# Optimization experiments

Measured on AMD Instinct MI355X. Metric: run time of the kernel, lower is better.

Reference implementation:

```python
import jax, jax.numpy as jnp
import numpy as np

N, E, D_IN, D_HID, D_OUT = 50000, 600000, 128, 128, 64


def setup_inputs() -> dict:
    key = jax.random.key(0)
    ks = jax.random.split(key, 8)
    x = jax.random.normal(ks[0], (N, D_IN), dtype=jnp.float32)
    edge_index = jax.random.randint(ks[1], (2, E), 0, N, dtype=jnp.int64)
    def glorot(k, fan_in, fan_out):
        s = (6.0 / (fan_in + fan_out)) ** 0.5
        return jax.random.uniform(k, (fan_in, fan_out), jnp.float32, -s, s)
    return {
        "x": x,
        "W1": glorot(ks[2], D_IN, D_HID), "b1": jnp.zeros((D_HID,), jnp.float32),
        "W2": glorot(ks[3], D_HID, D_HID), "b2": jnp.zeros((D_HID,), jnp.float32),
        "W3": glorot(ks[4], D_HID, D_OUT), "b3": jnp.zeros((D_OUT,), jnp.float32),
        "edge_index": edge_index,
    }


def reference(x, W1, b1, W2, b2, W3, b3, edge_index):
    n = x.shape[0]
    # GCN with self-loops: A_hat = A + I, norm = D^-1/2 A_hat D^-1/2
    loops = jnp.arange(n, dtype=edge_index.dtype)
    row = jnp.concatenate([edge_index[0], loops])  # source nodes
    col = jnp.concatenate([edge_index[1], loops])  # target nodes
    deg = jax.ops.segment_sum(jnp.ones_like(col, dtype=x.dtype), col, num_segments=n)
    dinv = jnp.where(deg > 0, jax.lax.rsqrt(deg), 0.0)
    norm = dinv[row] * dinv[col]  # [E+N]

    def gcn_conv(h, W, b):
        hw = h @ W                                   # [N, out]
        msg = hw[row] * norm[:, None]                # [E+N, out] gather + scale
        return jax.ops.segment_sum(msg, col, num_segments=n) + b

    h = jax.nn.relu(gcn_conv(x, W1, b1))
    h = jax.nn.relu(gcn_conv(h, W2, b2))
    return gcn_conv(h, W3, b3)
```

## Files before the change

kernel.cpp:

```cpp
#include <hip/hip_runtime.h>
#include <hip/hip_bf16.h>
#include <hip/hip_fp16.h>


typedef _Float16 h2 __attribute__((ext_vector_type(2)));
typedef _Float16 h8 __attribute__((ext_vector_type(8)));

__device__ inline float4 h4_to_f4(float2 raw) {
    __half2 lo = *reinterpret_cast<__half2*>(&raw.x);
    __half2 hi = *reinterpret_cast<__half2*>(&raw.y);
    float2 a = __half22float2(lo);
    float2 b = __half22float2(hi);
    return make_float4(a.x, a.y, b.x, b.y);
}

__device__ inline uint pack_h2(float a, float b) {
    __half2 h = __floats2half2_rn(a, b);
    return *reinterpret_cast<uint*>(&h);
}

__global__ __launch_bounds__(256) void zero_counts_kernel(int4* __restrict__ p, int n4) {
    int i = blockIdx.x * 256 + threadIdx.x;
    if (i < n4) p[i] = make_int4(0, 0, 0, 0);
}

__global__ __launch_bounds__(256) void f32_to_f16_kernel(const float4* __restrict__ in,
                                                         uint2* __restrict__ out, int n4) {
    int i = blockIdx.x * 256 + threadIdx.x;
    if (i < n4) {
        float4 v = in[i];
        out[i] = make_uint2(pack_h2(v.x, v.y), pack_h2(v.z, v.w));
    }
}

__global__ void count_edges_kernel(const int* __restrict__ col, int* __restrict__ counts, int E) {
    int e = blockIdx.x * blockDim.x + threadIdx.x;
    if (e < E) atomicAdd(&counts[col[e]], 1);
}

__global__ __launch_bounds__(256) void block_sum_kernel(const int* __restrict__ counts,
                                                        int* __restrict__ blocksum, int n) {
    int i = blockIdx.x * 256 + threadIdx.x;
    int v = (i < n) ? counts[i] : 0;
    #pragma unroll
    for (int d = 1; d < 64; d <<= 1) v += __shfl_xor(v, d);
    __shared__ int ws[4];
    if ((threadIdx.x & 63) == 0) ws[threadIdx.x >> 6] = v;
    __syncthreads();
    if (threadIdx.x == 0) blocksum[blockIdx.x] = ws[0] + ws[1] + ws[2] + ws[3];
}

__global__ __launch_bounds__(256) void scan_sums_kernel(const int* __restrict__ blocksum,
                                                        int* __restrict__ blockoff,
                                                        int* __restrict__ offsets, int nb, int n) {
    int tid = threadIdx.x;
    int lane = tid & 63, wid = tid >> 6;
    int orig = (tid < nb) ? blocksum[tid] : 0;
    int v = orig;
    #pragma unroll
    for (int d = 1; d < 64; d <<= 1) {
        int u = __shfl_up(v, d);
        if (lane >= d) v += u;
    }
    __shared__ int ws[4];
    if (lane == 63) ws[wid] = v;
    __syncthreads();
    int add = 0;
    for (int w = 0; w < wid; ++w) add += ws[w];
    v += add;
    if (tid < nb) blockoff[tid] = v - orig;
    if (tid == 255) offsets[n] = v;
}

__global__ __launch_bounds__(256) void write_offsets_kernel(const int* __restrict__ counts,
                                                            const int* __restrict__ blockoff,
                                                            int* __restrict__ offsets,
                                                            int* __restrict__ cursor,
                                                            float* __restrict__ dinv, int n) {
    int tid = threadIdx.x;
    int i = blockIdx.x * 256 + tid;
    int lane = tid & 63, wid = tid >> 6;
    int c = (i < n) ? counts[i] : 0;
    int v = c;
    #pragma unroll
    for (int d = 1; d < 64; d <<= 1) {
        int u = __shfl_up(v, d);
        if (lane >= d) v += u;
    }
    __shared__ int ws[4];
    if (lane == 63) ws[wid] = v;
    __syncthreads();
    int add = 0;
    for (int w = 0; w < wid; ++w) add += ws[w];
    int incl = v + add;
    if (i < n) {
        offsets[i] = blockoff[blockIdx.x] + incl - c;
        cursor[i] = 0;
        dinv[i] = rsqrtf((float)(c + 1));
    }
}

__global__ void fill_csr_kernel(const int* __restrict__ row, const int* __restrict__ col,
                                const int* __restrict__ offsets, int* __restrict__ cursor,
                                int* __restrict__ srcs, int E) {
    int e = blockIdx.x * blockDim.x + threadIdx.x;
    if (e < E) {
        int c = col[e];
        int pos = offsets[c] + atomicAdd(&cursor[c], 1);
        srcs[pos] = row[e];
    }
}

template <int DO>
__global__ __launch_bounds__(256) void gemm16_kernel(const __half* __restrict__ A,
                                                     const float* __restrict__ W,
                                                     const float* __restrict__ dinv,
                                                     __half* __restrict__ out, int n) {
    constexpr int K = 128;
    constexpr int COLTH = DO / 8;
    constexpr int ROWTH = 256 / COLTH;
    constexpr int R = 64 / ROWTH;
    constexpr int BR = ROWTH * R;
    constexpr int HALF = DO / 2;

    __shared__ alignas(16) h2 Wl[(K / 2) * DO];

    int tid = threadIdx.x;
    for (int idx = tid; idx < (K / 2) * (DO / 4); idx += 256) {
        int k2 = idx / (DO / 4);
        int c4 = idx % (DO / 4);
        float4 w0 = ((const float4*)(W + (size_t)(2 * k2) * DO))[c4];
        float4 w1 = ((const float4*)(W + (size_t)(2 * k2 + 1) * DO))[c4];
        h2* dst = &Wl[k2 * DO + c4 * 4];
        h2 d0; d0.x = (_Float16)w0.x; d0.y = (_Float16)w1.x; dst[0] = d0;
        h2 d1; d1.x = (_Float16)w0.y; d1.y = (_Float16)w1.y; dst[1] = d1;
        h2 d2; d2.x = (_Float16)w0.z; d2.y = (_Float16)w1.z; dst[2] = d2;
        h2 d3; d3.x = (_Float16)w0.w; d3.y = (_Float16)w1.w; dst[3] = d3;
    }
    __syncthreads();

    int ct = tid % COLTH;
    int rt = tid / COLTH;
    int rb = blockIdx.x * BR + rt * R;

    int rowc[R];
    #pragma unroll
    for (int i = 0; i < R; ++i) {
        int row = rb + i;
        rowc[i] = (row < n) ? row : (n - 1);
    }

    float acc[R][8];
    #pragma unroll
    for (int i = 0; i < R; ++i)
        #pragma unroll
        for (int c = 0; c < 8; ++c) acc[i][c] = 0.f;

    #pragma unroll 2
    for (int k8 = 0; k8 < K / 8; ++k8) {
        h8 av[R];
        #pragma unroll
        for (int i = 0; i < R; ++i) {
            av[i] = ((const h8*)(A + (size_t)rowc[i] * K))[k8];
        }
        #pragma unroll
        for (int kk = 0; kk < 4; ++kk) {
            int k2 = k8 * 4 + kk;
            h2 w0[4], w1[4];
            *(uint4*)w0 = *(const uint4*)(&Wl[k2 * DO + ct * 4]);
            *(uint4*)w1 = *(const uint4*)(&Wl[k2 * DO + HALF + ct * 4]);
            #pragma unroll
            for (int i = 0; i < R; ++i) {
                h2 a; a.x = av[i][2 * kk]; a.y = av[i][2 * kk + 1];
                #pragma unroll
                for (int c = 0; c < 4; ++c) {
                    acc[i][c]     = __builtin_amdgcn_fdot2(a, w0[c], acc[i][c], false);
                    acc[i][4 + c] = __builtin_amdgcn_fdot2(a, w1[c], acc[i][4 + c], false);
                }
            }
        }
    }

    #pragma unroll
    for (int i = 0; i < R; ++i) {
        int row = rb + i;
        if (row < n) {
            float dv = dinv[row];
            uint2 q0 = make_uint2(pack_h2(acc[i][0] * dv, acc[i][1] * dv),
                                  pack_h2(acc[i][2] * dv, acc[i][3] * dv));
            uint2 q1 = make_uint2(pack_h2(acc[i][4] * dv, acc[i][5] * dv),
                                  pack_h2(acc[i][6] * dv, acc[i][7] * dv));
            *(uint2*)(out + (size_t)row * DO + ct * 4) = q0;
            *(uint2*)(out + (size_t)row * DO + HALF + ct * 4) = q1;
        }
    }
}

template <int DO, bool RELU, bool F16OUT>
__global__ __launch_bounds__(256) void agg_kernel(const __half* __restrict__ hw,
                                                  const int* __restrict__ offsets,
                                                  const int* __restrict__ srcs,
                                                  const float* __restrict__ dinv,
                                                  const float* __restrict__ bias,
                                                  void* __restrict__ outp, int n) {
    constexpr int TPD = DO / 4;
    constexpr int DPB = 256 / TPD;
    int d = blockIdx.x * DPB + threadIdx.x / TPD;
    int j = threadIdx.x % TPD;
    if (d >= n) return;

    const float2* hw2 = (const float2*)hw;
    int beg = offsets[d];
    int end = offsets[d + 1];

    float4 acc = h4_to_f4(hw2[(size_t)d * TPD + j]);

    int e = beg;
    for (; e + 8 <= end; e += 8) {
        int s0 = srcs[e + 0], s1 = srcs[e + 1], s2 = srcs[e + 2], s3 = srcs[e + 3];
        int s4 = srcs[e + 4], s5 = srcs[e + 5], s6 = srcs[e + 6], s7 = srcs[e + 7];
        float4 v0 = h4_to_f4(hw2[(size_t)s0 * TPD + j]);
        float4 v1 = h4_to_f4(hw2[(size_t)s1 * TPD + j]);
        float4 v2 = h4_to_f4(hw2[(size_t)s2 * TPD + j]);
        float4 v3 = h4_to_f4(hw2[(size_t)s3 * TPD + j]);
        float4 v4 = h4_to_f4(hw2[(size_t)s4 * TPD + j]);
        float4 v5 = h4_to_f4(hw2[(size_t)s5 * TPD + j]);
        float4 v6 = h4_to_f4(hw2[(size_t)s6 * TPD + j]);
        float4 v7 = h4_to_f4(hw2[(size_t)s7 * TPD + j]);
        acc.x += v0.x; acc.y += v0.y; acc.z += v0.z; acc.w += v0.w;
        acc.x += v1.x; acc.y += v1.y; acc.z += v1.z; acc.w += v1.w;
        acc.x += v2.x; acc.y += v2.y; acc.z += v2.z; acc.w += v2.w;
        acc.x += v3.x; acc.y += v3.y; acc.z += v3.z; acc.w += v3.w;
        acc.x += v4.x; acc.y += v4.y; acc.z += v4.z; acc.w += v4.w;
        acc.x += v5.x; acc.y += v5.y; acc.z += v5.z; acc.w += v5.w;
        acc.x += v6.x; acc.y += v6.y; acc.z += v6.z; acc.w += v6.w;
        acc.x += v7.x; acc.y += v7.y; acc.z += v7.z; acc.w += v7.w;
    }
    for (; e + 4 <= end; e += 4) {
        int s0 = srcs[e + 0], s1 = srcs[e + 1], s2 = srcs[e + 2], s3 = srcs[e + 3];
        float4 v0 = h4_to_f4(hw2[(size_t)s0 * TPD + j]);
        float4 v1 = h4_to_f4(hw2[(size_t)s1 * TPD + j]);
        float4 v2 = h4_to_f4(hw2[(size_t)s2 * TPD + j]);
        float4 v3 = h4_to_f4(hw2[(size_t)s3 * TPD + j]);
        acc.x += v0.x; acc.y += v0.y; acc.z += v0.z; acc.w += v0.w;
        acc.x += v1.x; acc.y += v1.y; acc.z += v1.z; acc.w += v1.w;
        acc.x += v2.x; acc.y += v2.y; acc.z += v2.z; acc.w += v2.w;
        acc.x += v3.x; acc.y += v3.y; acc.z += v3.z; acc.w += v3.w;
    }
    for (; e < end; ++e) {
        float4 v = h4_to_f4(hw2[(size_t)srcs[e] * TPD + j]);
        acc.x += v.x; acc.y += v.y; acc.z += v.z; acc.w += v.w;
    }

    float di = dinv[d];
    float4 b4 = ((const float4*)bias)[j];
    acc.x = b4.x + di * acc.x;
    acc.y = b4.y + di * acc.y;
    acc.z = b4.z + di * acc.z;
    acc.w = b4.w + di * acc.w;

    if (RELU) {
        acc.x = fmaxf(acc.x, 0.f); acc.y = fmaxf(acc.y, 0.f);
        acc.z = fmaxf(acc.z, 0.f); acc.w = fmaxf(acc.w, 0.f);
    }
    if (F16OUT) {
        uint2 q = make_uint2(pack_h2(acc.x, acc.y), pack_h2(acc.z, acc.w));
        ((uint2*)outp)[(size_t)d * TPD + j] = q;
    } else {
        ((float4*)outp)[(size_t)d * TPD + j] = acc;
    }
}

extern "C" void kernel_launch(void* const* d_in, const int* in_sizes, int n_in,
                              void* d_out, int out_size, void* d_ws, size_t ws_size,
                              hipStream_t stream) {
    const float* x  = (const float*)d_in[0];
    const float* W1 = (const float*)d_in[1];
    const float* b1 = (const float*)d_in[2];
    const float* W2 = (const float*)d_in[3];
    const float* b2 = (const float*)d_in[4];
    const float* W3 = (const float*)d_in[5];
    const float* b3 = (const float*)d_in[6];
    const int*   ei = (const int*)d_in[7];

    const int N = in_sizes[0] / 128;
    const int E = in_sizes[7] / 2;
    const int* rowi = ei;
    const int* coli = ei + E;

    float* out = (float*)d_out;

    char* ws = (char*)d_ws;
    size_t off = 0;
    auto alloc = [&](size_t bytes) -> void* {
        void* p = ws + off;
        off = (off + bytes + 255) & ~(size_t)255;
        return p;
    };
    const int NB = (N + 255) / 256;
    float* dinv     = (float*)alloc((size_t)N * 4);
    int*   counts   = (int*)  alloc(((size_t)N + 4) * 4);
    int*   offsets  = (int*)  alloc((size_t)(N + 1) * 4);
    int*   cursor   = (int*)  alloc((size_t)N * 4);
    int*   blocksum = (int*)  alloc((size_t)NB * 4);
    int*   blockoff = (int*)  alloc((size_t)NB * 4);
    int*   srcs     = (int*)  alloc((size_t)E * 4);
    __half* x16     = (__half*)alloc((size_t)N * 128 * 2);
    __half* hw16    = (__half*)alloc((size_t)N * 128 * 2);
    __half* h16     = (__half*)alloc((size_t)N * 128 * 2);

    const int n4 = (N + 3) / 4;
    zero_counts_kernel<<<(n4 + 255) / 256, 256, 0, stream>>>((int4*)counts, n4);
    count_edges_kernel<<<(E + 255) / 256, 256, 0, stream>>>(coli, counts, E);
    block_sum_kernel<<<NB, 256, 0, stream>>>(counts, blocksum, N);
    scan_sums_kernel<<<1, 256, 0, stream>>>(blocksum, blockoff, offsets, NB, N);
    write_offsets_kernel<<<NB, 256, 0, stream>>>(counts, blockoff, offsets, cursor, dinv, N);
    fill_csr_kernel<<<(E + 255) / 256, 256, 0, stream>>>(rowi, coli, offsets, cursor, srcs, E);
    const int xc4 = N * 128 / 4;
    f32_to_f16_kernel<<<(xc4 + 255) / 256, 256, 0, stream>>>((const float4*)x, (uint2*)x16, xc4);

    gemm16_kernel<128><<<(N + 63) / 64, 256, 0, stream>>>(x16, W1, dinv, hw16, N);
    agg_kernel<128, true, true><<<(N + 7) / 8, 256, 0, stream>>>(hw16, offsets, srcs, dinv, b1, h16, N);

    gemm16_kernel<128><<<(N + 63) / 64, 256, 0, stream>>>(h16, W2, dinv, hw16, N);
    agg_kernel<128, true, true><<<(N + 7) / 8, 256, 0, stream>>>(hw16, offsets, srcs, dinv, b2, h16, N);

    gemm16_kernel<64><<<(N + 63) / 64, 256, 0, stream>>>(h16, W3, dinv, hw16, N);
    agg_kernel<64, false, false><<<(N + 15) / 16, 256, 0, stream>>>(hw16, offsets, srcs, dinv, b3, out, N);
}
```

Baseline: 215.7 us.

## Fuse prelude kernels, single-pass decoupled scan, and prefetch source indices in aggregation

Merges zeroing of the edge counts and the fp32-to-fp16 conversion of x into one kernel. Replaces the three-kernel offsets scan with a single-pass scan in which each block publishes its total to a flag slot and spins on all earlier slots. The aggregation loop now loads the next eight source indices while the current gathers are in flight. Together these cut the number of kernel launches and hide index-load latency, at the cost of relying on forward progress of earlier blocks for the spin-wait.

```diff
diff --git a/kernel.cpp b/kernel.cpp
--- a/kernel.cpp
+++ b/kernel.cpp
@@ -19,17 +19,17 @@
     return *reinterpret_cast<uint*>(&h);
 }
 
-__global__ __launch_bounds__(256) void zero_counts_kernel(int4* __restrict__ p, int n4) {
+__global__ __launch_bounds__(256) void prelude_init_kernel(const float4* __restrict__ x,
+                                                           uint2* __restrict__ x16,
+                                                           int4* __restrict__ counts4, int n4,
+                                                           int* __restrict__ aggslot, int nb,
+                                                           int xc4) {
     int i = blockIdx.x * 256 + threadIdx.x;
-    if (i < n4) p[i] = make_int4(0, 0, 0, 0);
-}
-
-__global__ __launch_bounds__(256) void f32_to_f16_kernel(const float4* __restrict__ in,
-                                                         uint2* __restrict__ out, int n4) {
-    int i = blockIdx.x * 256 + threadIdx.x;
-    if (i < n4) {
-        float4 v = in[i];
-        out[i] = make_uint2(pack_h2(v.x, v.y), pack_h2(v.z, v.w));
+    if (i < n4) counts4[i] = make_int4(0, 0, 0, 0);
+    if (i < nb) aggslot[i] = -1;
+    if (i < xc4) {
+        float4 v = x[i];
+        x16[i] = make_uint2(pack_h2(v.x, v.y), pack_h2(v.z, v.w));
     }
 }
 
@@ -38,66 +38,52 @@
     if (e < E) atomicAdd(&counts[col[e]], 1);
 }
 
-__global__ __launch_bounds__(256) void block_sum_kernel(const int* __restrict__ counts,
-                                                        int* __restrict__ blocksum, int n) {
-    int i = blockIdx.x * 256 + threadIdx.x;
-    int v = (i < n) ? counts[i] : 0;
-    #pragma unroll
-    for (int d = 1; d < 64; d <<= 1) v += __shfl_xor(v, d);
-    __shared__ int ws[4];
-    if ((threadIdx.x & 63) == 0) ws[threadIdx.x >> 6] = v;
-    __syncthreads();
-    if (threadIdx.x == 0) blocksum[blockIdx.x] = ws[0] + ws[1] + ws[2] + ws[3];
-}
-
-__global__ __launch_bounds__(256) void scan_sums_kernel(const int* __restrict__ blocksum,
-                                                        int* __restrict__ blockoff,
-                                                        int* __restrict__ offsets, int nb, int n) {
+__global__ __launch_bounds__(256) void scan_fused_kernel(const int* __restrict__ counts,
+                                                         int* __restrict__ aggslot,
+                                                         int* __restrict__ offsets,
+                                                         int* __restrict__ cursor,
+                                                         float* __restrict__ dinv, int n) {
+    int b = blockIdx.x;
     int tid = threadIdx.x;
     int lane = tid & 63, wid = tid >> 6;
-    int orig = (tid < nb) ? blocksum[tid] : 0;
-    int v = orig;
+    int i = b * 256 + tid;
+    int c = (i < n) ? counts[i] : 0;
+
+    int s = c;
     #pragma unroll
     for (int d = 1; d < 64; d <<= 1) {
-        int u = __shfl_up(v, d);
-        if (lane >= d) v += u;
+        int u = __shfl_up(s, d);
+        if (lane >= d) s += u;
     }
     __shared__ int ws[4];
-    if (lane == 63) ws[wid] = v;
+    if (lane == 63) ws[wid] = s;
     __syncthreads();
     int add = 0;
     for (int w = 0; w < wid; ++w) add += ws[w];
-    v += add;
-    if (tid < nb) blockoff[tid] = v - orig;
-    if (tid == 255) offsets[n] = v;
-}
-
-__global__ __launch_bounds__(256) void write_offsets_kernel(const int* __restrict__ counts,
-                                                            const int* __restrict__ blockoff,
-                                                            int* __restrict__ offsets,
-                                                            int* __restrict__ cursor,
-                                                            float* __restrict__ dinv, int n) {
-    int tid = threadIdx.x;
-    int i = blockIdx.x * 256 + tid;
-    int lane = tid & 63, wid = tid >> 6;
-    int c = (i < n) ? counts[i] : 0;
-    int v = c;
-    #pragma unroll
-    for (int d = 1; d < 64; d <<= 1) {
-        int u = __shfl_up(v, d);
-        if (lane >= d) v += u;
-    }
-    __shared__ int ws[4];
-    if (lane == 63) ws[wid] = v;
+    int incl = s + add;
+    int blocktotal = ws[0] + ws[1] + ws[2] + ws[3];
     __syncthreads();
-    int add = 0;
-    for (int w = 0; w < wid; ++w) add += ws[w];
-    int incl = v + add;
+
+    if (tid == 0) atomicExch(&aggslot[b], blocktotal);
+
+    int pre = 0;
+    for (int t = tid; t < b; t += 256) {
+        int a;
+        do { a = atomicAdd(&aggslot[t], 0); } while (a < 0);
+        pre += a;
+    }
+    #pragma unroll
+    for (int d = 1; d < 64; d <<= 1) pre += __shfl_xor(pre, d);
+    if (lane == 0) ws[wid] = pre;
+    __syncthreads();
+    int blockoff = ws[0] + ws[1] + ws[2] + ws[3];
+
     if (i < n) {
-        offsets[i] = blockoff[blockIdx.x] + incl - c;
+        offsets[i] = blockoff + incl - c;
         cursor[i] = 0;
         dinv[i] = rsqrtf((float)(c + 1));
     }
+    if (i == n - 1) offsets[n] = blockoff + incl;
 }
 
 __global__ void fill_csr_kernel(const int* __restrict__ row, const int* __restrict__ col,
@@ -216,25 +202,30 @@
     float4 acc = h4_to_f4(hw2[(size_t)d * TPD + j]);
 
     int e = beg;
-    for (; e + 8 <= end; e += 8) {
-        int s0 = srcs[e + 0], s1 = srcs[e + 1], s2 = srcs[e + 2], s3 = srcs[e + 3];
-        int s4 = srcs[e + 4], s5 = srcs[e + 5], s6 = srcs[e + 6], s7 = srcs[e + 7];
-        float4 v0 = h4_to_f4(hw2[(size_t)s0 * TPD + j]);
-        float4 v1 = h4_to_f4(hw2[(size_t)s1 * TPD + j]);
-        float4 v2 = h4_to_f4(hw2[(size_t)s2 * TPD + j]);
-        float4 v3 = h4_to_f4(hw2[(size_t)s3 * TPD + j]);
-        float4 v4 = h4_to_f4(hw2[(size_t)s4 * TPD + j]);
-        float4 v5 = h4_to_f4(hw2[(size_t)s5 * TPD + j]);
-        float4 v6 = h4_to_f4(hw2[(size_t)s6 * TPD + j]);
-        float4 v7 = h4_to_f4(hw2[(size_t)s7 * TPD + j]);
-        acc.x += v0.x; acc.y += v0.y; acc.z += v0.z; acc.w += v0.w;
-        acc.x += v1.x; acc.y += v1.y; acc.z += v1.z; acc.w += v1.w;
-        acc.x += v2.x; acc.y += v2.y; acc.z += v2.z; acc.w += v2.w;
-        acc.x += v3.x; acc.y += v3.y; acc.z += v3.z; acc.w += v3.w;
-        acc.x += v4.x; acc.y += v4.y; acc.z += v4.z; acc.w += v4.w;
-        acc.x += v5.x; acc.y += v5.y; acc.z += v5.z; acc.w += v5.w;
-        acc.x += v6.x; acc.y += v6.y; acc.z += v6.z; acc.w += v6.w;
-        acc.x += v7.x; acc.y += v7.y; acc.z += v7.z; acc.w += v7.w;
+    if (e + 8 <= end) {
+        int cs[8];
+        #pragma unroll
+        for (int k = 0; k < 8; ++k) cs[k] = srcs[e + k];
+        while (true) {
+            float2 g[8];
+            #pragma unroll
+            for (int k = 0; k < 8; ++k) g[k] = hw2[(size_t)cs[k] * TPD + j];
+            e += 8;
+            bool more = (e + 8 <= end);
+            int nx[8];
+            if (more) {
+                #pragma unroll
+                for (int k = 0; k < 8; ++k) nx[k] = srcs[e + k];
+            }
+            #pragma unroll
+            for (int k = 0; k < 8; ++k) {
+                float4 f = h4_to_f4(g[k]);
+                acc.x += f.x; acc.y += f.y; acc.z += f.z; acc.w += f.w;
+            }
+            if (!more) break;
+            #pragma unroll
+            for (int k = 0; k < 8; ++k) cs[k] = nx[k];
+        }
     }
     for (; e + 4 <= end; e += 4) {
         int s0 = srcs[e + 0], s1 = srcs[e + 1], s2 = srcs[e + 2], s3 = srcs[e + 3];
@@ -302,22 +293,19 @@
     int*   counts   = (int*)  alloc(((size_t)N + 4) * 4);
     int*   offsets  = (int*)  alloc((size_t)(N + 1) * 4);
     int*   cursor   = (int*)  alloc((size_t)N * 4);
-    int*   blocksum = (int*)  alloc((size_t)NB * 4);
-    int*   blockoff = (int*)  alloc((size_t)NB * 4);
+    int*   aggslot  = (int*)  alloc((size_t)NB * 4);
     int*   srcs     = (int*)  alloc((size_t)E * 4);
     __half* x16     = (__half*)alloc((size_t)N * 128 * 2);
     __half* hw16    = (__half*)alloc((size_t)N * 128 * 2);
     __half* h16     = (__half*)alloc((size_t)N * 128 * 2);
 
     const int n4 = (N + 3) / 4;
-    zero_counts_kernel<<<(n4 + 255) / 256, 256, 0, stream>>>((int4*)counts, n4);
+    const int xc4 = N * 128 / 4;
+    prelude_init_kernel<<<(xc4 + 255) / 256, 256, 0, stream>>>(
+        (const float4*)x, (uint2*)x16, (int4*)counts, n4, aggslot, NB, xc4);
     count_edges_kernel<<<(E + 255) / 256, 256, 0, stream>>>(coli, counts, E);
-    block_sum_kernel<<<NB, 256, 0, stream>>>(counts, blocksum, N);
-    scan_sums_kernel<<<1, 256, 0, stream>>>(blocksum, blockoff, offsets, NB, N);
-    write_offsets_kernel<<<NB, 256, 0, stream>>>(counts, blockoff, offsets, cursor, dinv, N);
+    scan_fused_kernel<<<NB, 256, 0, stream>>>(counts, aggslot, offsets, cursor, dinv, N);
     fill_csr_kernel<<<(E + 255) / 256, 256, 0, stream>>>(rowi, coli, offsets, cursor, srcs, E);
-    const int xc4 = N * 128 / 4;
-    f32_to_f16_kernel<<<(xc4 + 255) / 256, 256, 0, stream>>>((const float4*)x, (uint2*)x16, xc4);
 
     gemm16_kernel<128><<<(N + 63) / 64, 256, 0, stream>>>(x16, W1, dinv, hw16, N);
     agg_kernel<128, true, true><<<(N + 7) / 8, 256, 0, stream>>>(hw16, offsets, srcs, dinv, b1, h16, N);
```

Measured after the change: 211.0 us. 2.2% less time.
